# Optimization experiments

Hardware: AMD Instinct MI355X
Metric: run time of the kernel (lower is better)

The kernel has to match this reference:

```python
import jax, jax.numpy as jnp
import numpy as np
import math

B, S, D, H, L = 256, 256, 256, 4, 2
DH = D // H
NITEMS = 50000
EPS = 1e-5


def setup_inputs() -> dict:
    key = jax.random.key(0)
    ks = jax.random.split(key, 16)
    w = lambda k, shape, scale: (jax.random.normal(k, shape, jnp.float32) * scale)
    return {
        "input_ids": jax.random.randint(ks[0], (B, S), 0, NITEMS),
        "item_emb": w(ks[1], (NITEMS, D), 0.02),
        "pos_emb": w(ks[2], (S, D), 0.02),
        "Wq": w(ks[3], (L, D, D), 0.05),
        "bq": jnp.zeros((L, D), jnp.float32),
        "Wk": w(ks[4], (L, D, D), 0.05),
        "bk": jnp.zeros((L, D), jnp.float32),
        "Wv": w(ks[5], (L, D, D), 0.05),
        "bv": jnp.zeros((L, D), jnp.float32),
        "Wo": w(ks[6], (L, D, D), 0.05),
        "bo": jnp.zeros((L, D), jnp.float32),
        "W1": w(ks[7], (L, D, 4 * D), 0.05),
        "b1": jnp.zeros((L, 4 * D), jnp.float32),
        "W2": w(ks[8], (L, 4 * D, D), 0.05),
        "b2": jnp.zeros((L, D), jnp.float32),
    }


def _layer_norm(x):
    mu = jnp.mean(x, axis=-1, keepdims=True)
    var = jnp.mean(jnp.square(x - mu), axis=-1, keepdims=True)
    return (x - mu) * jax.lax.rsqrt(var + EPS)


def reference(input_ids, item_emb, pos_emb, Wq, bq, Wk, bk, Wv, bv,
              Wo, bo, W1, b1, W2, b2):
    Bn, Sn = input_ids.shape
    dtype = item_emb.dtype
    # attention bias: padding (id>0) AND causal; (1-mask)*-10000
    pad = (input_ids > 0).astype(dtype)                       # [B,S]
    causal = jnp.tril(jnp.ones((Sn, Sn), dtype))              # [S,S]
    mask = pad[:, None, None, :] * causal[None, None]         # [B,1,S,S]
    attn_bias = (1.0 - mask) * -10000.0

    # input embedding (dropout is identity in eval)
    x = _layer_norm(item_emb[input_ids] + pos_emb[None])      # [B,S,D]
    total = x
    scale = 1.0 / math.sqrt(DH)

    for l in range(L):
        # --- self-attention ---
        def heads(z):  # [B,S,D] -> [B,H,S,DH]
            return z.reshape(Bn, Sn, H, DH).transpose(0, 2, 1, 3)
        q = heads(x @ Wq[l] + bq[l])
        k = heads(x @ Wk[l] + bk[l])
        v = heads(x @ Wv[l] + bv[l])
        scores = jnp.einsum('bhqd,bhkd->bhqk', q, k) * scale + attn_bias
        probs = jax.nn.softmax(scores, axis=-1)
        ctx = jnp.einsum('bhqk,bhkd->bhqd', probs, v)
        ctx = ctx.transpose(0, 2, 1, 3).reshape(Bn, Sn, D)
        h = _layer_norm(ctx @ Wo[l] + bo[l] + x)
        # --- FFN (no residual in IntermediateLayer) ---
        ffn = jax.nn.gelu(h @ W1[l] + b1[l], approximate=False) @ W2[l] + b2[l]
        x = _layer_norm(ffn)
        total = total + x

    return total
```

## Files before the change

kernel.cpp:

```cpp
#include <hip/hip_runtime.h>
#include <math.h>

typedef __attribute__((ext_vector_type(8))) short short8;
typedef __attribute__((ext_vector_type(4))) short shortx4;
typedef __attribute__((ext_vector_type(4))) float floatx4;

#define BQ 256
#define SQ 256
#define DQ 256
#define HQ 4

__device__ __forceinline__ short f2bf(float f) {
  union { float f; unsigned u; } c; c.f = f;
  unsigned r = c.u + 0x7fffu + ((c.u >> 16) & 1u);
  return (short)(r >> 16);
}
__device__ __forceinline__ float bf2f(short s) {
  union { unsigned u; float f; } c; c.u = ((unsigned)(unsigned short)s) << 16;
  return c.f;
}
__device__ __forceinline__ float gelu_fast(float x) {
  float t = x * (0.7978845608f + 0.0356774081f * x * x);
  return x / (1.0f + __expf(-2.0f * t));
}
__device__ __forceinline__ void async16(const void* g, void* l) {
  __builtin_amdgcn_global_load_lds(
      (const __attribute__((address_space(1))) void*)g,
      (__attribute__((address_space(3))) void*)l, 16, 0, 0);
}

__global__ __launch_bounds__(256) void wtrans_kernel(
    const float* __restrict__ Wq, const float* __restrict__ Wk, const float* __restrict__ Wv,
    const float* __restrict__ Wo, const float* __restrict__ W1, const float* __restrict__ W2,
    const float* __restrict__ bq, const float* __restrict__ bk, const float* __restrict__ bv,
    short* __restrict__ WqkvT, short* __restrict__ WoT, short* __restrict__ W1T,
    short* __restrict__ W2T, float* __restrict__ bqkv) {
  const int bid = blockIdx.x, tid = threadIdx.x;
  if (bid >= 384) {
    int i = bid - 384;
    int l = i / 3, which = i - l * 3;
    const float* src = (which == 0) ? bq : ((which == 1) ? bk : bv);
    bqkv[l * 768 + which * 256 + tid] = src[l * 256 + tid];
    return;
  }
  __shared__ float t[64][65];
  const float* src; short* dst; int K, N, tile;
  if (bid < 96)       { int l = bid / 48, r = bid % 48, which = r / 16; tile = r % 16;
    src = ((which == 0) ? Wq : (which == 1) ? Wk : Wv) + l * 65536;
    dst = WqkvT + (l * 3 + which) * 65536; K = 256; N = 256; }
  else if (bid < 128) { int i = bid - 96, l = i / 16; tile = i % 16;
    src = Wo + l * 65536; dst = WoT + l * 65536; K = 256; N = 256; }
  else if (bid < 256) { int i = bid - 128, l = i / 64; tile = i % 64;
    src = W1 + l * 262144; dst = W1T + l * 262144; K = 256; N = 1024; }
  else                { int i = bid - 256, l = i / 64; tile = i % 64;
    src = W2 + l * 262144; dst = W2T + l * 262144; K = 1024; N = 256; }
  const int ntj = N >> 6;
  const int ti = tile / ntj, tj = tile - ti * ntj;
  {
    int r = tid >> 2, c0 = (tid & 3) * 16;
    const float* sp = src + (size_t)(ti * 64 + r) * N + tj * 64 + c0;
#pragma unroll
    for (int j = 0; j < 4; ++j) {
      floatx4 v = *(const floatx4*)(sp + j * 4);
      t[r][c0 + j * 4 + 0] = v[0]; t[r][c0 + j * 4 + 1] = v[1];
      t[r][c0 + j * 4 + 2] = v[2]; t[r][c0 + j * 4 + 3] = v[3];
    }
  }
  __syncthreads();
  {
    int d = tid & 63, ch = tid >> 6;
    short8 o[2];
#pragma unroll
    for (int j = 0; j < 16; ++j) o[j >> 3][j & 7] = f2bf(t[ch * 16 + j][d]);
    short* dp = dst + (size_t)(tj * 64 + d) * K + ti * 64 + ch * 16;
    *(short8*)dp = o[0];
    *(short8*)(dp + 8) = o[1];
  }
}

__global__ __launch_bounds__(256) void embed_kernel(const int* __restrict__ ids,
    const float* __restrict__ item, const float* __restrict__ pos,
    short* __restrict__ xb, float* __restrict__ tot) {
  const int tid = threadIdx.x, lane = tid & 63, w = tid >> 6;
  const int row = blockIdx.x * 4 + w;
  const int s = row & (SQ - 1);
  const int id = ids[row];
  floatx4 a = *(const floatx4*)(item + (size_t)id * DQ + lane * 4);
  floatx4 p = *(const floatx4*)(pos + (size_t)s * DQ + lane * 4);
  float v[4];
#pragma unroll
  for (int i = 0; i < 4; ++i) v[i] = a[i] + p[i];
  float sm = v[0] + v[1] + v[2] + v[3];
  float ss = v[0]*v[0] + v[1]*v[1] + v[2]*v[2] + v[3]*v[3];
#pragma unroll
  for (int off = 32; off; off >>= 1) { sm += __shfl_xor(sm, off); ss += __shfl_xor(ss, off); }
  float mu = sm * (1.0f / DQ);
  float var = ss * (1.0f / DQ) - mu * mu;
  float rs = rsqrtf(var + 1e-5f);
  shortx4 o; floatx4 y;
#pragma unroll
  for (int i = 0; i < 4; ++i) { y[i] = (v[i] - mu) * rs; o[i] = f2bf(y[i]); }
  *(shortx4*)(xb + (size_t)row * DQ + lane * 4) = o;
  *(floatx4*)(tot + (size_t)row * DQ + lane * 4) = y;
}

template <int ACT, int LN, int RES, int TOT, int SMODE>
__global__ __launch_bounds__(512, 4) void gemm_kernel(
    const short* __restrict__ A, const short* __restrict__ Bt,
    const float* __restrict__ bias, const short* __restrict__ res,
    short* __restrict__ out, float* __restrict__ tot, short* __restrict__ vt,
    int M, int N, int K) {
  __shared__ short smem[26624];
  float* redS  = (float*)(smem + 24576);
  float* redS2 = redS + 512;
  const int tid = threadIdx.x, lane = tid & 63, w = tid >> 6;
  const int lane15 = lane & 15, quad = lane >> 4;
  const int wm = w & 1, wn = w >> 1;

  const int gx = gridDim.x;
  const int nwg = gx * gridDim.y;
  const int orig = blockIdx.y * gx + blockIdx.x;
  const int chunk = nwg >> 3;
  const int sw = (orig & 7) * chunk + (orig >> 3);
  const int bm = sw / gx, bn = sw - bm * gx;

  const int rA = lane >> 2;
  const int swzA = (rA & 3) ^ ((rA >> 2) & 3);
  const int gA = ((lane & 3) ^ swzA) * 8;
  const short* Ag  = A  + (size_t)(bm * 128 + w * 16 + rA) * K + gA;
  const short* Bg0 = Bt + (size_t)(bn * 256 + w * 32 + rA) * K + gA;
  const short* Bg1 = Bg0 + (size_t)16 * K;
  const int qs = ((quad ^ ((lane15 & 3) ^ ((lane15 >> 2) & 3))) * 8);

  floatx4 acc[4][4] = {};
  const int nk = K >> 5;
#define GSTG(kb_)                                                        \
  do {                                                                   \
    short* As_ = smem + (((kb_) & 1) * 12288);                           \
    async16(Ag  + (kb_) * 32, &As_[w * 512]);                            \
    async16(Bg0 + (kb_) * 32, &As_[4096 + w * 1024]);                    \
    async16(Bg1 + (kb_) * 32, &As_[4096 + w * 1024 + 512]);              \
  } while (0)

  GSTG(0);
  for (int kb = 0; kb < nk; ++kb) {
    __syncthreads();
    if (kb + 1 < nk) GSTG(kb + 1);
    const short* Asb = smem + ((kb & 1) * 12288);
    const short* Bsb = Asb + 4096;
    short8 af[4], bfr[4];
#pragma unroll
    for (int i = 0; i < 4; ++i) {
      af[i]  = *(const short8*)&Asb[(wm * 64 + i * 16 + lane15) * 32 + qs];
      bfr[i] = *(const short8*)&Bsb[(wn * 64 + i * 16 + lane15) * 32 + qs];
    }
#pragma unroll
    for (int i = 0; i < 4; ++i)
#pragma unroll
      for (int j = 0; j < 4; ++j)
        acc[i][j] = __builtin_amdgcn_mfma_f32_16x16x32_bf16(bfr[j], af[i], acc[i][j], 0, 0, 0);
  }
#undef GSTG

  float sum_[4], sq_[4];
#pragma unroll
  for (int i = 0; i < 4; ++i) { sum_[i] = 0.0f; sq_[i] = 0.0f; }
#pragma unroll
  for (int i = 0; i < 4; ++i) {
    size_t rowg = (size_t)bm * 128 + wm * 64 + i * 16 + lane15;
#pragma unroll
    for (int j = 0; j < 4; ++j) {
      int nloc = wn * 64 + j * 16 + quad * 4;
      floatx4 b4 = *(const floatx4*)(bias + bn * 256 + nloc);
      shortx4 r4;
      if (RES) r4 = *(const shortx4*)(res + rowg * 256 + nloc);
#pragma unroll
      for (int r = 0; r < 4; ++r) {
        float z = acc[i][j][r] + b4[r];
        if (RES) z += bf2f(r4[r]);
        if (ACT) z = gelu_fast(z);
        acc[i][j][r] = z;
        if (LN) { sum_[i] += z; sq_[i] += z * z; }
      }
    }
  }

  if (LN) {
#pragma unroll
    for (int i = 0; i < 4; ++i) {
      sum_[i] += __shfl_xor(sum_[i], 16); sum_[i] += __shfl_xor(sum_[i], 32);
      sq_[i]  += __shfl_xor(sq_[i], 16);  sq_[i]  += __shfl_xor(sq_[i], 32);
    }
    if (quad == 0) {
#pragma unroll
      for (int i = 0; i < 4; ++i) {
        int lr = wm * 64 + i * 16 + lane15;
        redS[lr * 4 + wn] = sum_[i];
        redS2[lr * 4 + wn] = sq_[i];
      }
    }
    __syncthreads();
#pragma unroll
    for (int i = 0; i < 4; ++i) {
      int lr = wm * 64 + i * 16 + lane15;
      float s = redS[lr * 4] + redS[lr * 4 + 1] + redS[lr * 4 + 2] + redS[lr * 4 + 3];
      float q = redS2[lr * 4] + redS2[lr * 4 + 1] + redS2[lr * 4 + 2] + redS2[lr * 4 + 3];
      float mu = s * (1.0f / 256.0f);
      float var = q * (1.0f / 256.0f) - mu * mu;
      float rs = rsqrtf(var + 1e-5f);
      size_t rowg = (size_t)bm * 128 + wm * 64 + i * 16 + lane15;
#pragma unroll
      for (int j = 0; j < 4; ++j) {
        int nloc = wn * 64 + j * 16 + quad * 4;
        floatx4 y;
#pragma unroll
        for (int r = 0; r < 4; ++r) y[r] = (acc[i][j][r] - mu) * rs;
        acc[i][j] = y;
        if (TOT) {
          floatx4* tp = (floatx4*)(tot + rowg * 256 + nloc);
          floatx4 t = *tp;
#pragma unroll
          for (int r = 0; r < 4; ++r) t[r] += y[r];
          *tp = t;
        }
      }
    }
  }

#pragma unroll
  for (int i = 0; i < 4; ++i) {
    __syncthreads();
    int lr = wm * 16 + lane15;
#pragma unroll
    for (int j = 0; j < 4; ++j) {
      shortx4 o;
#pragma unroll
      for (int r = 0; r < 4; ++r) o[r] = f2bf(acc[i][j][r]);
      *(shortx4*)&smem[lr * 264 + wn * 64 + j * 16 + quad * 4] = o;
    }
    __syncthreads();
    if (SMODE == 1 && bn == 2) {
      int d = tid & 255;
      int grp = tid >> 8;
      short vv[16];
#pragma unroll
      for (int rr = 0; rr < 16; ++rr) vv[rr] = smem[(grp * 16 + rr) * 264 + d];
      size_t row = ((size_t)((bm >> 1) * 256 + d)) * 256 + (bm & 1) * 128 + grp * 64 + i * 16;
      *(short8*)(vt + row) = *(short8*)&vv[0];
      *(short8*)(vt + row + 8) = *(short8*)&vv[8];
    } else {
#pragma unroll
      for (int it = 0; it < 2; ++it) {
        int t2 = tid + it * 512;
        int lr2 = t2 >> 5, c = (t2 & 31) * 8;
        short8 v = *(const short8*)&smem[lr2 * 264 + c];
        size_t rowg = (size_t)bm * 128 + (lr2 >> 4) * 64 + i * 16 + (lr2 & 15);
        short* dst = (SMODE == 1) ? out + (size_t)bn * M * 256 + rowg * 256 + c
                                  : out + rowg * (size_t)N + bn * 256 + c;
        *(short8*)dst = v;
      }
    }
  }
}

__global__ __launch_bounds__(512, 4) void attn_kernel(
    const short* __restrict__ qg, const short* __restrict__ kg,
    const short* __restrict__ vtg, const int* __restrict__ ids,
    short* __restrict__ ctxg) {
  __shared__ short lds[25088];
  float* padS = (float*)&lds[24576];
  const int tid = threadIdx.x, lane = tid & 63, w = tid >> 6;
  const int lane15 = lane & 15, quad = lane >> 4, l7 = lane15 & 7;
  const int h = blockIdx.x & 3, b = blockIdx.x >> 2;

  if (tid < 256) padS[tid] = (ids[b * 256 + tid] > 0) ? 0.0f : -10000.0f;

  const int stA[2] = {w, 15 - w};
  short8 qf[2][2];
#pragma unroll
  for (int tt = 0; tt < 2; ++tt) {
    int q0 = stA[tt] * 16;
#pragma unroll
    for (int ks = 0; ks < 2; ++ks)
      qf[tt][ks] = *(const short8*)(qg + (size_t)(b * 256 + q0 + lane15) * 256 +
                                    h * 64 + ks * 32 + quad * 8);
  }

  float m_[2][4], l_[2][4];
  floatx4 o[2][4];
#pragma unroll
  for (int tt = 0; tt < 2; ++tt)
#pragma unroll
    for (int r = 0; r < 4; ++r) {
      m_[tt][r] = -1e30f; l_[tt][r] = 0.0f;
#pragma unroll
      for (int dt = 0; dt < 4; ++dt) o[tt][dt][r] = 0.0f;
    }

  const int srow = tid >> 3;
  const int g8 = ((tid & 7) ^ (srow & 7)) * 8;
  const short* kgp = kg + (size_t)(b * 256 + srow) * 256 + h * 64 + g8;
  const short* vgp = vtg + (size_t)(b * 256 + h * 64 + srow) * 256 + g8;
  short* pbuf = &lds[16384 + w * 1024];

#define STG(kb_, ib_)                                                     \
  do {                                                                    \
    async16(kgp + (size_t)(kb_) * 64 * 256, &lds[(ib_) * 4096 + w * 512]);\
    async16(vgp + (kb_) * 64, &lds[8192 + (ib_) * 4096 + w * 512]);       \
  } while (0)

  STG(0, 0);

  for (int kb = 0; kb < 4; ++kb) {
    __syncthreads();
    if (kb < 3) STG(kb + 1, (kb + 1) & 1);
    const short* kbuf = &lds[(kb & 1) * 4096];
    const short* vbuf = &lds[8192 + (kb & 1) * 4096];

#pragma unroll
    for (int tt = 0; tt < 2; ++tt) {
      const int st = stA[tt];
      if (st < 4 * kb) continue;
      const int q0 = st * 16;
      const int diag = (st >> 2) == kb;
      const int stlo = st & 3;
      floatx4 e[4];
#pragma unroll
      for (int t16 = 0; t16 < 4; ++t16) {
        if (diag && t16 > stlo) {
          e[t16] = (floatx4){-1e30f, -1e30f, -1e30f, -1e30f};
          continue;
        }
        floatx4 a = {0.f, 0.f, 0.f, 0.f};
#pragma unroll
        for (int ks = 0; ks < 2; ++ks) {
          short8 kf = *(const short8*)&kbuf[(t16 * 16 + lane15) * 64 +
                                            (((ks * 4 + quad) ^ l7) * 8)];
          a = __builtin_amdgcn_mfma_f32_16x16x32_bf16(qf[tt][ks], kf, a, 0, 0, 0);
        }
        float pb = padS[kb * 64 + t16 * 16 + lane15];
        if (diag && t16 == stlo) {
          int kk = kb * 64 + t16 * 16 + lane15;
#pragma unroll
          for (int r = 0; r < 4; ++r)
            e[t16][r] = a[r] * 0.125f + ((kk <= q0 + quad * 4 + r) ? pb : -10000.0f);
        } else {
#pragma unroll
          for (int r = 0; r < 4; ++r) e[t16][r] = a[r] * 0.125f + pb;
        }
      }
#pragma unroll
      for (int r = 0; r < 4; ++r) {
        float mx = fmaxf(fmaxf(e[0][r], e[1][r]), fmaxf(e[2][r], e[3][r]));
        mx = fmaxf(mx, __shfl_xor(mx, 1)); mx = fmaxf(mx, __shfl_xor(mx, 2));
        mx = fmaxf(mx, __shfl_xor(mx, 4)); mx = fmaxf(mx, __shfl_xor(mx, 8));
        float mn = fmaxf(m_[tt][r], mx);
        float alpha = __expf(m_[tt][r] - mn);
        m_[tt][r] = mn;
        float s = 0.0f;
#pragma unroll
        for (int t16 = 0; t16 < 4; ++t16) {
          float ev = __expf(e[t16][r] - mn);
          e[t16][r] = ev; s += ev;
        }
        s += __shfl_xor(s, 1); s += __shfl_xor(s, 2);
        s += __shfl_xor(s, 4); s += __shfl_xor(s, 8);
        l_[tt][r] = l_[tt][r] * alpha + s;
#pragma unroll
        for (int dt = 0; dt < 4; ++dt) o[tt][dt][r] *= alpha;
        int qloc = quad * 4 + r;
        int swq = (qloc & 7) ^ (qloc >> 2);
#pragma unroll
        for (int t16 = 0; t16 < 4; ++t16) {
          int slot = (t16 * 2 + (lane15 >> 3)) ^ swq;
          pbuf[qloc * 64 + slot * 8 + l7] = f2bf(e[t16][r]);
        }
      }
#pragma unroll
      for (int kb2 = 0; kb2 < 2; ++kb2) {
        short8 pf = *(const short8*)&pbuf[lane15 * 64 +
                      (((kb2 * 4 + quad) ^ l7 ^ (lane15 >> 2)) * 8)];
#pragma unroll
        for (int dt = 0; dt < 4; ++dt) {
          short8 vf = *(const short8*)&vbuf[(dt * 16 + lane15) * 64 +
                        (((kb2 * 4 + quad) ^ l7) * 8)];
          o[tt][dt] = __builtin_amdgcn_mfma_f32_16x16x32_bf16(pf, vf, o[tt][dt], 0, 0, 0);
        }
      }
    }
  }

#pragma unroll
  for (int tt = 0; tt < 2; ++tt) {
    const int q0 = stA[tt] * 16;
#pragma unroll
    for (int r = 0; r < 4; ++r) {
      int qloc = quad * 4 + r;
      float inv = 1.0f / l_[tt][r];
#pragma unroll
      for (int dt = 0; dt < 4; ++dt)
        pbuf[qloc * 64 + ((dt ^ quad) * 16) + lane15] = f2bf(o[tt][dt][r] * inv);
    }
#pragma unroll
    for (int it = 0; it < 2; ++it) {
      int idx = it * 64 + lane;
      int row = idx >> 3, u = idx & 7;
      int d0 = (((u >> 1) ^ (row >> 2)) << 4) + (u & 1) * 8;
      short8 v = *(const short8*)&pbuf[row * 64 + u * 8];
      *(short8*)(ctxg + (size_t)(b * 256 + q0 + row) * 256 + h * 64 + d0) = v;
    }
  }
}

extern "C" void kernel_launch(void* const* d_in, const int* in_sizes, int n_in,
                              void* d_out, int out_size, void* d_ws, size_t ws_size,
                              hipStream_t stream) {
  const int*   ids  = (const int*)d_in[0];
  const float* item = (const float*)d_in[1];
  const float* pos  = (const float*)d_in[2];
  const float* Wq = (const float*)d_in[3];  const float* bq = (const float*)d_in[4];
  const float* Wk = (const float*)d_in[5];  const float* bk = (const float*)d_in[6];
  const float* Wv = (const float*)d_in[7];  const float* bv = (const float*)d_in[8];
  const float* Wo = (const float*)d_in[9];  const float* bo = (const float*)d_in[10];
  const float* W1 = (const float*)d_in[11]; const float* b1 = (const float*)d_in[12];
  const float* W2 = (const float*)d_in[13]; const float* b2 = (const float*)d_in[14];
  float* out = (float*)d_out;

  const size_t EL = (size_t)BQ * SQ * DQ;
  short* qb    = (short*)d_ws;
  short* kb_   = qb + EL;
  short* vt    = kb_ + EL;
  short* ctxb  = vt + EL;
  short* gb    = qb;
  short* xb    = ctxb + EL;
  short* hb    = xb + EL;
  short* WqkvT = hb + EL;
  short* WoT   = WqkvT + 2 * 3 * 65536;
  short* W1T   = WoT + 2 * 65536;
  short* W2T   = W1T + 2 * 262144;
  float* bqkv  = (float*)(W2T + 2 * 262144);

  const int M = BQ * SQ;

  wtrans_kernel<<<390, 256, 0, stream>>>(Wq, Wk, Wv, Wo, W1, W2, bq, bk, bv,
                                         WqkvT, WoT, W1T, W2T, bqkv);
  embed_kernel<<<M / 4, 256, 0, stream>>>(ids, item, pos, xb, out);

  for (int l = 0; l < 2; ++l) {
    gemm_kernel<0, 0, 0, 0, 1><<<dim3(3, M / 128), 512, 0, stream>>>(
        xb, WqkvT + (size_t)l * 3 * 65536, bqkv + l * 768, nullptr, qb, nullptr, vt,
        M, 768, 256);
    attn_kernel<<<BQ * HQ, 512, 0, stream>>>(qb, kb_, vt, ids, ctxb);
    gemm_kernel<0, 1, 1, 0, 0><<<dim3(1, M / 128), 512, 0, stream>>>(
        ctxb, WoT + (size_t)l * 65536, bo + l * 256, xb, hb, nullptr, nullptr,
        M, 256, 256);
    gemm_kernel<1, 0, 0, 0, 0><<<dim3(4, M / 128), 512, 0, stream>>>(
        hb, W1T + (size_t)l * 262144, b1 + l * 1024, nullptr, gb, nullptr, nullptr,
        M, 1024, 256);
    gemm_kernel<0, 1, 0, 1, 0><<<dim3(1, M / 128), 512, 0, stream>>>(
        gb, W2T + (size_t)l * 262144, b2 + l * 256, nullptr, xb, out, nullptr,
        M, 256, 1024);
  }
}
```

Measured before the change: 804.9 us.

## Split attention blocks by query half and read K/V directly from global

The attention kernel now launches twice as many 256-thread blocks, each covering half the query tiles and visiting only the causally needed key blocks. K and V fragments are loaded straight from global memory, replacing the async double-buffered LDS staging and barriers. The padding mask is built with a wave ballot rather than an LDS table. This cuts LDS use and synchronisation to raise occupancy, but K/V reuse across waves now depends on the cache, and the two block types carry unequal work.

```diff
diff --git a/kernel.cpp b/kernel.cpp
--- a/kernel.cpp
+++ b/kernel.cpp
@@ -263,19 +263,17 @@
   }
 }
 
-__global__ __launch_bounds__(512, 4) void attn_kernel(
+__global__ __launch_bounds__(256) void attn_kernel(
     const short* __restrict__ qg, const short* __restrict__ kg,
     const short* __restrict__ vtg, const int* __restrict__ ids,
     short* __restrict__ ctxg) {
-  __shared__ short lds[25088];
-  float* padS = (float*)&lds[24576];
+  __shared__ short lds[4096];
   const int tid = threadIdx.x, lane = tid & 63, w = tid >> 6;
   const int lane15 = lane & 15, quad = lane >> 4, l7 = lane15 & 7;
-  const int h = blockIdx.x & 3, b = blockIdx.x >> 2;
-
-  if (tid < 256) padS[tid] = (ids[b * 256 + tid] > 0) ? 0.0f : -10000.0f;
-
-  const int stA[2] = {w, 15 - w};
+  const int hh = blockIdx.x & 1, bh = blockIdx.x >> 1;
+  const int h = bh & 3, b = bh >> 2;
+
+  const int stA[2] = {hh * 8 + w, hh * 8 + 7 - w};
   short8 qf[2][2];
 #pragma unroll
   for (int tt = 0; tt < 2; ++tt) {
@@ -297,25 +295,14 @@
       for (int dt = 0; dt < 4; ++dt) o[tt][dt][r] = 0.0f;
     }
 
-  const int srow = tid >> 3;
-  const int g8 = ((tid & 7) ^ (srow & 7)) * 8;
-  const short* kgp = kg + (size_t)(b * 256 + srow) * 256 + h * 64 + g8;
-  const short* vgp = vtg + (size_t)(b * 256 + h * 64 + srow) * 256 + g8;
-  short* pbuf = &lds[16384 + w * 1024];
-
-#define STG(kb_, ib_)                                                     \
-  do {                                                                    \
-    async16(kgp + (size_t)(kb_) * 64 * 256, &lds[(ib_) * 4096 + w * 512]);\
-    async16(vgp + (kb_) * 64, &lds[8192 + (ib_) * 4096 + w * 512]);       \
-  } while (0)
-
-  STG(0, 0);
-
-  for (int kb = 0; kb < 4; ++kb) {
-    __syncthreads();
-    if (kb < 3) STG(kb + 1, (kb + 1) & 1);
-    const short* kbuf = &lds[(kb & 1) * 4096];
-    const short* vbuf = &lds[8192 + (kb & 1) * 4096];
+  short* pbuf = &lds[w * 1024];
+  const short* kbase0 = kg + (size_t)(b * 256) * 256 + h * 64;
+  const short* vbase  = vtg + (size_t)(b * 256 + h * 64) * 256;
+
+  const int nkb = hh ? 4 : 2;
+  for (int kb = 0; kb < nkb; ++kb) {
+    const unsigned long long pm = __ballot(ids[b * 256 + kb * 64 + lane] > 0);
+    const short* kbase = kbase0 + (size_t)(kb * 64) * 256;
 
 #pragma unroll
     for (int tt = 0; tt < 2; ++tt) {
@@ -334,11 +321,11 @@
         floatx4 a = {0.f, 0.f, 0.f, 0.f};
 #pragma unroll
         for (int ks = 0; ks < 2; ++ks) {
-          short8 kf = *(const short8*)&kbuf[(t16 * 16 + lane15) * 64 +
-                                            (((ks * 4 + quad) ^ l7) * 8)];
+          short8 kf = *(const short8*)(kbase + (size_t)(t16 * 16 + lane15) * 256 +
+                                       ks * 32 + quad * 8);
           a = __builtin_amdgcn_mfma_f32_16x16x32_bf16(qf[tt][ks], kf, a, 0, 0, 0);
         }
-        float pb = padS[kb * 64 + t16 * 16 + lane15];
+        float pb = ((pm >> (t16 * 16 + lane15)) & 1ull) ? 0.0f : -10000.0f;
         if (diag && t16 == stlo) {
           int kk = kb * 64 + t16 * 16 + lane15;
 #pragma unroll
@@ -382,8 +369,8 @@
                       (((kb2 * 4 + quad) ^ l7 ^ (lane15 >> 2)) * 8)];
 #pragma unroll
         for (int dt = 0; dt < 4; ++dt) {
-          short8 vf = *(const short8*)&vbuf[(dt * 16 + lane15) * 64 +
-                        (((kb2 * 4 + quad) ^ l7) * 8)];
+          short8 vf = *(const short8*)(vbase + (size_t)(dt * 16 + lane15) * 256 +
+                                       kb * 64 + kb2 * 32 + quad * 8);
           o[tt][dt] = __builtin_amdgcn_mfma_f32_16x16x32_bf16(pf, vf, o[tt][dt], 0, 0, 0);
         }
       }
@@ -450,7 +437,7 @@
     gemm_kernel<0, 0, 0, 0, 1><<<dim3(3, M / 128), 512, 0, stream>>>(
         xb, WqkvT + (size_t)l * 3 * 65536, bqkv + l * 768, nullptr, qb, nullptr, vt,
         M, 768, 256);
-    attn_kernel<<<BQ * HQ, 512, 0, stream>>>(qb, kb_, vt, ids, ctxb);
+    attn_kernel<<<BQ * HQ * 2, 256, 0, stream>>>(qb, kb_, vt, ids, ctxb);
     gemm_kernel<0, 1, 1, 0, 0><<<dim3(1, M / 128), 512, 0, stream>>>(
         ctxb, WoT + (size_t)l * 65536, bo + l * 256, xb, hb, nullptr, nullptr,
         M, 256, 256);
```

Result: no change. 811.5 us (+0.8%).

## Add 128x128-tile GEMM kernel for QKV and FFN1 projections

Applied to the files above, without the earlier changes.

Adds a separate 256-thread GEMM kernel with 128x128 output tiles and double-buffered async loads, used for the QKV and W1 (GELU) projections in place of the 512-thread 128x256 kernel. The smaller tile doubles the number of workgroups and cuts LDS use per block, which should raise occupancy and balance across CUs. The cost is lower operand reuse per tile and more redundant A-tile loads. The V-transpose epilogue is moved into the new kernel and removed from the old one.

```diff
diff --git a/kernel.cpp b/kernel.cpp
--- a/kernel.cpp
+++ b/kernel.cpp
@@ -104,6 +104,114 @@
   *(floatx4*)(tot + (size_t)row * DQ + lane * 4) = y;
 }
 
+template <int ACT, int SMODE>
+__global__ __launch_bounds__(256, 4) void gemm128_kernel(
+    const short* __restrict__ A, const short* __restrict__ Bt,
+    const float* __restrict__ bias, short* __restrict__ out, short* __restrict__ vt,
+    int M, int N, int K) {
+  __shared__ short smem[16384];
+  const int tid = threadIdx.x, lane = tid & 63, w = tid >> 6;
+  const int lane15 = lane & 15, quad = lane >> 4;
+  const int wm = w & 1, wn = w >> 1;
+
+  const int gx = gridDim.x;
+  const int nwg = gx * gridDim.y;
+  const int orig = blockIdx.y * gx + blockIdx.x;
+  const int chunk = nwg >> 3;
+  const int sw = (orig & 7) * chunk + (orig >> 3);
+  const int bm = sw / gx, bn = sw - bm * gx;
+
+  const int rA = lane >> 2;
+  const int swzA = (rA & 3) ^ ((rA >> 2) & 3);
+  const int gA = ((lane & 3) ^ swzA) * 8;
+  const short* Ag  = A  + (size_t)(bm * 128 + w * 16 + rA) * K + gA;
+  const short* Ag2 = Ag + (size_t)64 * K;
+  const short* Bg0 = Bt + (size_t)(bn * 128 + w * 16 + rA) * K + gA;
+  const short* Bg1 = Bg0 + (size_t)64 * K;
+  const int qs = ((quad ^ ((lane15 & 3) ^ ((lane15 >> 2) & 3))) * 8);
+
+  floatx4 acc[4][4] = {};
+  const int nk = K >> 5;
+#define GSTG2(kb_)                                                       \
+  do {                                                                   \
+    short* S = smem + (((kb_) & 1) * 8192);                              \
+    async16(Ag  + (kb_) * 32, &S[w * 512]);                              \
+    async16(Ag2 + (kb_) * 32, &S[2048 + w * 512]);                       \
+    async16(Bg0 + (kb_) * 32, &S[4096 + w * 512]);                       \
+    async16(Bg1 + (kb_) * 32, &S[6144 + w * 512]);                       \
+  } while (0)
+
+  GSTG2(0);
+  for (int kb = 0; kb < nk; ++kb) {
+    __syncthreads();
+    if (kb + 1 < nk) GSTG2(kb + 1);
+    const short* Asb = smem + ((kb & 1) * 8192);
+    const short* Bsb = Asb + 4096;
+    short8 af[4], bfr[4];
+#pragma unroll
+    for (int i = 0; i < 4; ++i) {
+      af[i]  = *(const short8*)&Asb[(wm * 64 + i * 16 + lane15) * 32 + qs];
+      bfr[i] = *(const short8*)&Bsb[(wn * 64 + i * 16 + lane15) * 32 + qs];
+    }
+#pragma unroll
+    for (int i = 0; i < 4; ++i)
+#pragma unroll
+      for (int j = 0; j < 4; ++j)
+        acc[i][j] = __builtin_amdgcn_mfma_f32_16x16x32_bf16(bfr[j], af[i], acc[i][j], 0, 0, 0);
+  }
+#undef GSTG2
+
+#pragma unroll
+  for (int i = 0; i < 4; ++i)
+#pragma unroll
+    for (int j = 0; j < 4; ++j) {
+      int nloc = wn * 64 + j * 16 + quad * 4;
+      floatx4 b4 = *(const floatx4*)(bias + bn * 128 + nloc);
+#pragma unroll
+      for (int r = 0; r < 4; ++r) {
+        float z = acc[i][j][r] + b4[r];
+        if (ACT) z = gelu_fast(z);
+        acc[i][j][r] = z;
+      }
+    }
+
+#pragma unroll
+  for (int i = 0; i < 4; ++i) {
+    __syncthreads();
+    int lr = wm * 16 + lane15;
+#pragma unroll
+    for (int j = 0; j < 4; ++j) {
+      shortx4 o;
+#pragma unroll
+      for (int r = 0; r < 4; ++r) o[r] = f2bf(acc[i][j][r]);
+      *(shortx4*)&smem[lr * 132 + wn * 64 + j * 16 + quad * 4] = o;
+    }
+    __syncthreads();
+    if (SMODE == 1 && bn >= 4) {
+      int d = tid & 127, grp = tid >> 7;
+      short vv[16];
+#pragma unroll
+      for (int rr = 0; rr < 16; ++rr) vv[rr] = smem[(grp * 16 + rr) * 132 + d];
+      size_t row = ((size_t)((bm >> 1) * 256 + (bn - 4) * 128 + d)) * 256 +
+                   (bm & 1) * 128 + grp * 64 + i * 16;
+      *(short8*)(vt + row) = *(short8*)&vv[0];
+      *(short8*)(vt + row + 8) = *(short8*)&vv[8];
+    } else {
+#pragma unroll
+      for (int it = 0; it < 2; ++it) {
+        int t2 = tid + it * 256;
+        int lr2 = t2 >> 4, c = (t2 & 15) * 8;
+        short8 v = *(const short8*)&smem[lr2 * 132 + c];
+        size_t rowg = (size_t)bm * 128 + (lr2 >> 4) * 64 + i * 16 + (lr2 & 15);
+        short* dst = (SMODE == 1)
+            ? out + (size_t)(bn >> 1) * M * 256 + rowg * 256 + (bn & 1) * 128 + c
+            : out + rowg * (size_t)N + bn * 128 + c;
+        *(short8*)dst = v;
+      }
+    }
+  }
+}
+
 template <int ACT, int LN, int RES, int TOT, int SMODE>
 __global__ __launch_bounds__(512, 4) void gemm_kernel(
     const short* __restrict__ A, const short* __restrict__ Bt,
@@ -239,26 +347,14 @@
       *(shortx4*)&smem[lr * 264 + wn * 64 + j * 16 + quad * 4] = o;
     }
     __syncthreads();
-    if (SMODE == 1 && bn == 2) {
-      int d = tid & 255;
-      int grp = tid >> 8;
-      short vv[16];
-#pragma unroll
-      for (int rr = 0; rr < 16; ++rr) vv[rr] = smem[(grp * 16 + rr) * 264 + d];
-      size_t row = ((size_t)((bm >> 1) * 256 + d)) * 256 + (bm & 1) * 128 + grp * 64 + i * 16;
-      *(short8*)(vt + row) = *(short8*)&vv[0];
-      *(short8*)(vt + row + 8) = *(short8*)&vv[8];
-    } else {
-#pragma unroll
-      for (int it = 0; it < 2; ++it) {
-        int t2 = tid + it * 512;
-        int lr2 = t2 >> 5, c = (t2 & 31) * 8;
-        short8 v = *(const short8*)&smem[lr2 * 264 + c];
-        size_t rowg = (size_t)bm * 128 + (lr2 >> 4) * 64 + i * 16 + (lr2 & 15);
-        short* dst = (SMODE == 1) ? out + (size_t)bn * M * 256 + rowg * 256 + c
-                                  : out + rowg * (size_t)N + bn * 256 + c;
-        *(short8*)dst = v;
-      }
+#pragma unroll
+    for (int it = 0; it < 2; ++it) {
+      int t2 = tid + it * 512;
+      int lr2 = t2 >> 5, c = (t2 & 31) * 8;
+      short8 v = *(const short8*)&smem[lr2 * 264 + c];
+      size_t rowg = (size_t)bm * 128 + (lr2 >> 4) * 64 + i * 16 + (lr2 & 15);
+      short* dst = out + rowg * (size_t)N + bn * 256 + c;
+      *(short8*)dst = v;
     }
   }
 }
@@ -447,16 +543,14 @@
   embed_kernel<<<M / 4, 256, 0, stream>>>(ids, item, pos, xb, out);
 
   for (int l = 0; l < 2; ++l) {
-    gemm_kernel<0, 0, 0, 0, 1><<<dim3(3, M / 128), 512, 0, stream>>>(
-        xb, WqkvT + (size_t)l * 3 * 65536, bqkv + l * 768, nullptr, qb, nullptr, vt,
-        M, 768, 256);
+    gemm128_kernel<0, 1><<<dim3(6, M / 128), 256, 0, stream>>>(
+        xb, WqkvT + (size_t)l * 3 * 65536, bqkv + l * 768, qb, vt, M, 768, 256);
     attn_kernel<<<BQ * HQ, 512, 0, stream>>>(qb, kb_, vt, ids, ctxb);
     gemm_kernel<0, 1, 1, 0, 0><<<dim3(1, M / 128), 512, 0, stream>>>(
         ctxb, WoT + (size_t)l * 65536, bo + l * 256, xb, hb, nullptr, nullptr,
         M, 256, 256);
-    gemm_kernel<1, 0, 0, 0, 0><<<dim3(4, M / 128), 512, 0, stream>>>(
-        hb, W1T + (size_t)l * 262144, b1 + l * 1024, nullptr, gb, nullptr, nullptr,
-        M, 1024, 256);
+    gemm128_kernel<1, 0><<<dim3(8, M / 128), 256, 0, stream>>>(
+        hb, W1T + (size_t)l * 262144, b1 + l * 1024, gb, nullptr, M, 1024, 256);
     gemm_kernel<0, 1, 0, 1, 0><<<dim3(1, M / 128), 512, 0, stream>>>(
         gb, W2T + (size_t)l * 262144, b2 + l * 256, nullptr, xb, out, nullptr,
         M, 256, 1024);
```

New measurement: 780.5 us. 3.0% less time.
